# Kernel tuning notes

Measured on AMD Instinct MI355X. Metric: run time of the kernel, lower is better.

## Reference

```python
import jax, jax.numpy as jnp
import numpy as np
import math

NUM_POINTS = 64
OUTPUT_DIMS = 128
MINVAL = -1.0
MAXVAL = 1.0
WINDOW_SIZE = 8.0


def setup_inputs() -> dict:
    key = jax.random.key(0)
    k1, k2 = jax.random.split(key)
    # continuous feature values in [minval, maxval]
    x = jax.random.uniform(k1, (64, 8192), dtype=jnp.float32, minval=MINVAL, maxval=MAXVAL)
    embeddings = jax.random.normal(k2, (NUM_POINTS, OUTPUT_DIMS), dtype=jnp.float32)
    return {"x": x, "embeddings": embeddings}


def _rect_window(d, window_size):
    w_2 = window_size / 2
    return (jnp.sign(d + w_2) - jnp.sign(d - w_2)) * 0.5


def _hann_window(d, window_size):
    y = jnp.cos(jnp.float32(math.pi) * d / window_size)
    return y * y * _rect_window(d, window_size)


def reference(x, embeddings):
    # map x from [minval, maxval] to grid coordinates [0, num_points]
    scale = jnp.float32(NUM_POINTS / (MAXVAL - MINVAL))
    xs = (x - jnp.float32(MINVAL)) * scale
    points = jnp.arange(NUM_POINTS, dtype=jnp.float32)
    # [B, S, num_points] distance to each grid point
    d = xs[..., None] - points
    w = _hann_window(d, jnp.float32(WINDOW_SIZE))
    # normalized: divide_no_nan semantics (0 where row-sum == 0)
    s = jnp.sum(w, axis=-1, keepdims=True)
    w = jnp.where(s == 0, jnp.float32(0), w / jnp.where(s == 0, jnp.float32(1), s))
    # [B, S, output_dims]
    return jnp.einsum('bsp,pd->bsd', w, embeddings)
```

## Files before the change

kernel.cpp:

```cpp
#include <hip/hip_runtime.h>
#include <math.h>

#define NUM_POINTS 64
#define OUT_DIMS 128
#define BLOCK_THREADS 256
#define ELEMS_PER_BLOCK 256

__global__ __launch_bounds__(BLOCK_THREADS) void ce_kernel(
    const float* __restrict__ x,
    const float* __restrict__ emb,
    float* __restrict__ out) {
  __shared__ float s_emb[NUM_POINTS * OUT_DIMS];
  {
    float4* s4 = (float4*)s_emb;
    const float4* e4 = (const float4*)emb;
    const int t = threadIdx.x;
#pragma unroll
    for (int i = 0; i < (NUM_POINTS * OUT_DIMS / 4) / BLOCK_THREADS; ++i)
      s4[t + i * BLOCK_THREADS] = e4[t + i * BLOCK_THREADS];
  }
  __syncthreads();

  const int tid = threadIdx.x;
  const int lane_chunk = tid & 31;
  const int sub = tid >> 5;
  const int base = blockIdx.x * ELEMS_PER_BLOCK;

#pragma unroll 1
  for (int it = 0; it < ELEMS_PER_BLOCK / 8; ++it) {
    const int e = base + it * 8 + sub;
    const float xv = x[e];
    const float xs = (xv + 1.0f) * 32.0f;
    const int p0 = (int)floorf(xs) - 3;

    float w[8];
    float wsum = 0.0f;
#pragma unroll
    for (int j = 0; j < 8; ++j) {
      const int p = p0 + j;
      const float d = xs - (float)p;
      const float c = __builtin_amdgcn_cosf(d * 0.0625f);
      float wv = c * c;
      wv = (p >= 0 && p < NUM_POINTS) ? wv : 0.0f;
      w[j] = wv;
      wsum += wv;
    }
    const float inv = (wsum != 0.0f) ? __builtin_amdgcn_rcpf(wsum) : 0.0f;
#pragma unroll
    for (int j = 0; j < 8; ++j) w[j] *= inv;

    float4 acc = make_float4(0.f, 0.f, 0.f, 0.f);
#pragma unroll
    for (int j = 0; j < 8; ++j) {
      int p = p0 + j;
      p = (p < 0) ? 0 : ((p > NUM_POINTS - 1) ? NUM_POINTS - 1 : p);
      const float4 ev = ((const float4*)(s_emb + p * OUT_DIMS))[lane_chunk];
      acc.x = fmaf(w[j], ev.x, acc.x);
      acc.y = fmaf(w[j], ev.y, acc.y);
      acc.z = fmaf(w[j], ev.z, acc.z);
      acc.w = fmaf(w[j], ev.w, acc.w);
    }
    ((float4*)(out + (size_t)e * OUT_DIMS))[lane_chunk] = acc;
  }
}

extern "C" void kernel_launch(void* const* d_in, const int* in_sizes, int n_in,
                              void* d_out, int out_size, void* d_ws, size_t ws_size,
                              hipStream_t stream) {
  const float* x = (const float*)d_in[0];
  const float* emb = (const float*)d_in[1];
  float* out = (float*)d_out;

  const int n = in_sizes[0];
  const int blocks = n / ELEMS_PER_BLOCK;
  ce_kernel<<<blocks, BLOCK_THREADS, 0, stream>>>(x, emb, out);
}
```

Before: 299.3 us.

## Precompute per-element Hann weights once per thread into shared memory

Window weights and clamped start indices are now computed once per element, one element per thread, and stored in shared memory, instead of being recomputed redundantly by all 32 lanes of each sub-group. The main loop then reads the weights and offset from LDS and does 8 row FMAs from contiguous embedding rows, unrolled by 2. This removes about 32x redundant cos/rcp work and per-iteration global loads of x. The cost is 9 KB of extra LDS per block, which may reduce occupancy. The kernel is likely bound by output writes (256 MB), so the gain may be limited.

```diff
diff --git a/kernel.cpp b/kernel.cpp
--- a/kernel.cpp
+++ b/kernel.cpp
@@ -11,56 +11,69 @@
     const float* __restrict__ emb,
     float* __restrict__ out) {
   __shared__ float s_emb[NUM_POINTS * OUT_DIMS];
+  __shared__ __align__(16) float s_w[ELEMS_PER_BLOCK * 8];
+  __shared__ int s_p0[ELEMS_PER_BLOCK];
+
+  const int t = threadIdx.x;
+  const int base = blockIdx.x * ELEMS_PER_BLOCK;
+
   {
     float4* s4 = (float4*)s_emb;
     const float4* e4 = (const float4*)emb;
-    const int t = threadIdx.x;
 #pragma unroll
     for (int i = 0; i < (NUM_POINTS * OUT_DIMS / 4) / BLOCK_THREADS; ++i)
       s4[t + i * BLOCK_THREADS] = e4[t + i * BLOCK_THREADS];
   }
-  __syncthreads();
 
-  const int tid = threadIdx.x;
-  const int lane_chunk = tid & 31;
-  const int sub = tid >> 5;
-  const int base = blockIdx.x * ELEMS_PER_BLOCK;
-
-#pragma unroll 1
-  for (int it = 0; it < ELEMS_PER_BLOCK / 8; ++it) {
-    const int e = base + it * 8 + sub;
-    const float xv = x[e];
+  {
+    const float xv = x[base + t];
     const float xs = (xv + 1.0f) * 32.0f;
-    const int p0 = (int)floorf(xs) - 3;
-
+    int p0 = (int)floorf(xs) - 3;
+    int p0c = p0 < 0 ? 0 : (p0 > NUM_POINTS - 8 ? NUM_POINTS - 8 : p0);
     float w[8];
     float wsum = 0.0f;
 #pragma unroll
     for (int j = 0; j < 8; ++j) {
-      const int p = p0 + j;
-      const float d = xs - (float)p;
+      const float d = xs - (float)(p0c + j);
       const float c = __builtin_amdgcn_cosf(d * 0.0625f);
       float wv = c * c;
-      wv = (p >= 0 && p < NUM_POINTS) ? wv : 0.0f;
+      wv = (d > -4.0f && d < 4.0f) ? wv : 0.0f;
       w[j] = wv;
       wsum += wv;
     }
     const float inv = (wsum != 0.0f) ? __builtin_amdgcn_rcpf(wsum) : 0.0f;
 #pragma unroll
     for (int j = 0; j < 8; ++j) w[j] *= inv;
+    float4* wp = (float4*)&s_w[t * 8];
+    wp[0] = make_float4(w[0], w[1], w[2], w[3]);
+    wp[1] = make_float4(w[4], w[5], w[6], w[7]);
+    s_p0[t] = p0c;
+  }
+  __syncthreads();
+
+  const int lane_chunk = t & 31;
+  const int sub = t >> 5;
+
+#pragma unroll 2
+  for (int it = 0; it < ELEMS_PER_BLOCK / 8; ++it) {
+    const int slot = it * 8 + sub;
+    const int p0c = s_p0[slot];
+    const float4* wp = (const float4*)&s_w[slot * 8];
+    const float4 wa = wp[0];
+    const float4 wb = wp[1];
+    const float* rowp = s_emb + p0c * OUT_DIMS + lane_chunk * 4;
 
     float4 acc = make_float4(0.f, 0.f, 0.f, 0.f);
+    const float wj[8] = {wa.x, wa.y, wa.z, wa.w, wb.x, wb.y, wb.z, wb.w};
 #pragma unroll
     for (int j = 0; j < 8; ++j) {
-      int p = p0 + j;
-      p = (p < 0) ? 0 : ((p > NUM_POINTS - 1) ? NUM_POINTS - 1 : p);
-      const float4 ev = ((const float4*)(s_emb + p * OUT_DIMS))[lane_chunk];
-      acc.x = fmaf(w[j], ev.x, acc.x);
-      acc.y = fmaf(w[j], ev.y, acc.y);
-      acc.z = fmaf(w[j], ev.z, acc.z);
-      acc.w = fmaf(w[j], ev.w, acc.w);
+      const float4 ev = *(const float4*)(rowp + j * OUT_DIMS);
+      acc.x = fmaf(wj[j], ev.x, acc.x);
+      acc.y = fmaf(wj[j], ev.y, acc.y);
+      acc.z = fmaf(wj[j], ev.z, acc.z);
+      acc.w = fmaf(wj[j], ev.w, acc.w);
     }
-    ((float4*)(out + (size_t)e * OUT_DIMS))[lane_chunk] = acc;
+    ((float4*)(out + (size_t)(base + slot) * OUT_DIMS))[lane_chunk] = acc;
   }
 }
 
```

Result: no change. 303.1 us (+1.3%).
